# Performance work log

Measured on AMD Instinct MI355X. Metric: run time of the kernel, lower is better.

## Reference

```python
import jax, jax.numpy as jnp
import numpy as np

N, E, F_IN, D, H = 20000, 640000, 128, 16, 8  # nodes, edges, in_features, out_features, n_heads


def _linear_params(k, fan_in, fan_out):
    W = jax.random.normal(k, (fan_in, fan_out), jnp.float32) / np.sqrt(fan_in)
    b = jnp.zeros((fan_out,), jnp.float32)
    return W, b


def setup_inputs() -> dict:
    key = jax.random.key(0)
    ks = jax.random.split(key, 8)
    x = jax.random.normal(ks[0], (N, F_IN), jnp.float32)
    edge_index = jax.random.randint(ks[1], (2, E), 0, N, dtype=jnp.int64)
    Wq, bq = _linear_params(ks[2], F_IN, D * H)
    Wk, bk = _linear_params(ks[3], F_IN, D * H)
    Wv, bv = _linear_params(ks[4], F_IN, D * H)
    Wpsi, bpsi = _linear_params(ks[5], D, D)
    Wo, bo = _linear_params(ks[6], D * H * 2, F_IN)
    gamma = jnp.ones((F_IN,), jnp.float32)
    beta = jnp.zeros((F_IN,), jnp.float32)
    return {"x": x, "edge_index": edge_index, "Wq": Wq, "bq": bq, "Wk": Wk, "bk": bk,
            "Wv": Wv, "bv": bv, "Wpsi": Wpsi, "bpsi": bpsi, "Wo": Wo, "bo": bo,
            "gamma": gamma, "beta": beta}


def _segment_softmax(logits, seg, num_segments):
    # numerically-stable softmax of edge logits grouped by destination node (row)
    m = jax.ops.segment_max(logits, seg, num_segments=num_segments)  # [N,H]
    m = jnp.where(jnp.isfinite(m), m, 0.0)
    e = jnp.exp(logits - m[seg])  # [E,H]
    s = jax.ops.segment_sum(e, seg, num_segments=num_segments)  # [N,H]
    return e / (s[seg] + 1e-16)


def reference(x, edge_index, Wq, bq, Wk, bk, Wv, bv, Wpsi, bpsi, Wo, bo, gamma, beta):
    q = (x @ Wq + bq).reshape(N, H, D)
    k = (x @ Wk + bk).reshape(N, H, D)
    v = (x @ Wv + bv).reshape(N, H, D)
    row, col = edge_index[0], edge_index[1]

    logits = jnp.einsum('ehd,ehd->eh', q[row], k[col]) / np.sqrt(D)  # [E,H]
    alpha = _segment_softmax(logits, row, N)  # [E,H]

    v_j = v[col]  # [E,H,D]
    h_lp = jax.ops.segment_sum((alpha[..., None] * v_j).reshape(E, H * D), row, num_segments=N)
    v_bp = jnp.tanh(v_j @ Wpsi + bpsi)  # per-head linear on last dim, [E,H,D]
    h_bp = jax.ops.segment_sum((alpha[..., None] * v_bp).reshape(E, H * D), row, num_segments=N)

    h_out = jnp.concatenate([h_lp, h_bp], axis=1) @ Wo + bo  # [N,F_IN]
    y = x + jax.nn.relu(h_out)
    mu = jnp.mean(y, axis=-1, keepdims=True)
    var = jnp.mean(jnp.square(y - mu), axis=-1, keepdims=True)
    return (y - mu) * jax.lax.rsqrt(var + 1e-5) * gamma + beta
```

## Files before the change

### kernel.cpp

```cpp
#include <hip/hip_runtime.h>
#include <hip/hip_bf16.h>
#include <math.h>

#define NN 20000
#define EE 640000

typedef __attribute__((ext_vector_type(8))) short short8;
typedef __attribute__((ext_vector_type(4))) float f32x4;
typedef __hip_bfloat16 bf16;
typedef __hip_bfloat162 bf162;

__device__ inline ushort f2bf(float f) {
  bf16 h = __float2bfloat16(f);
  return *(ushort*)&h;
}
__device__ inline float2 bf2u(uint u) {
  return __bfloat1622float2(*(const bf162*)&u);
}
__device__ inline float fast_tanh(float x) {
  float xx = fminf(fmaxf(x, -9.0f), 9.0f);
  float e = exp2f(xx * 2.885390082f);
  return (e - 1.0f) * __builtin_amdgcn_rcpf(e + 1.0f);
}
__device__ inline short8 frag_from_f32(const float* p) {
  float4 f0 = *(const float4*)p;
  float4 f1 = *(const float4*)(p + 4);
  ushort tmp[8] = {f2bf(f0.x), f2bf(f0.y), f2bf(f0.z), f2bf(f0.w),
                   f2bf(f1.x), f2bf(f1.y), f2bf(f1.z), f2bf(f1.w)};
  return *(const short8*)tmp;
}


__global__ __launch_bounds__(256, 4) void qkv_gemm(
    const float* __restrict__ x,
    const float* __restrict__ Wq, const float* __restrict__ bq,
    const float* __restrict__ Wk, const float* __restrict__ bk,
    const float* __restrict__ Wv, const float* __restrict__ bv,
    float* __restrict__ qbuf,
    ushort* __restrict__ kbuf, ushort* __restrict__ vbuf) {
  __shared__ ushort WB[128 * 136];
  int t = threadIdx.x;
  int n0 = blockIdx.x * 128;
  int mat = blockIdx.y;
  const float* W    = mat == 0 ? Wq : (mat == 1 ? Wk : Wv);
  const float* bias = mat == 0 ? bq : (mat == 1 ? bk : bv);

  {
    int k = t >> 1, nh = (t & 1) * 64;
    const float* src = W + (size_t)k * 128 + nh;
#pragma unroll
    for (int i = 0; i < 16; ++i) {
      float4 f = *(const float4*)(src + 4 * i);
      WB[(nh + 4 * i + 0) * 136 + k] = f2bf(f.x);
      WB[(nh + 4 * i + 1) * 136 + k] = f2bf(f.y);
      WB[(nh + 4 * i + 2) * 136 + k] = f2bf(f.z);
      WB[(nh + 4 * i + 3) * 136 + k] = f2bf(f.w);
    }
  }
  __syncthreads();

  int w = t >> 6, lane = t & 63;
  int m = lane & 15, q = lane >> 4;
  int r0 = w * 32;
  int row0 = n0 + r0 + m;
  int row1 = row0 + 16;
  bool ok0 = row0 < NN, ok1 = row1 < NN;
  const float* xr0 = x + (size_t)row0 * 128;
  const float* xr1 = x + (size_t)row1 * 128;
  const short8 z8 = (short8){0, 0, 0, 0, 0, 0, 0, 0};

  f32x4 acc0[8], acc1[8];
#pragma unroll
  for (int c = 0; c < 8; ++c) {
    acc0[c] = (f32x4){0.f, 0.f, 0.f, 0.f};
    acc1[c] = (f32x4){0.f, 0.f, 0.f, 0.f};
  }
#pragma unroll
  for (int kt = 0; kt < 4; ++kt) {
    int kof = kt * 32 + 8 * q;
    short8 a0 = ok0 ? frag_from_f32(xr0 + kof) : z8;
    short8 a1 = ok1 ? frag_from_f32(xr1 + kof) : z8;
#pragma unroll
    for (int c = 0; c < 8; ++c) {
      short8 b = *(const short8*)&WB[(c * 16 + m) * 136 + kof];
      acc0[c] = __builtin_amdgcn_mfma_f32_16x16x32_bf16(a0, b, acc0[c], 0, 0, 0);
      acc1[c] = __builtin_amdgcn_mfma_f32_16x16x32_bf16(a1, b, acc1[c], 0, 0, 0);
    }
  }
  if (mat == 0) {
#pragma unroll
    for (int c = 0; c < 8; ++c) {
      int col = c * 16 + m;
      float bb = bias[col];
#pragma unroll
      for (int reg = 0; reg < 4; ++reg) {
        int ra = n0 + r0 + 4 * q + reg;
        int rb = ra + 16;
        if (ra < NN) qbuf[(size_t)ra * 128 + col] = acc0[c][reg] + bb;
        if (rb < NN) qbuf[(size_t)rb * 128 + col] = acc1[c][reg] + bb;
      }
    }
  } else {
    ushort* dst = (mat == 1) ? kbuf : vbuf;
#pragma unroll
    for (int c = 0; c < 8; ++c) {
      int col = c * 16 + m;
      float bb = bias[col];
#pragma unroll
      for (int reg = 0; reg < 4; ++reg) {
        int ra = n0 + r0 + 4 * q + reg;
        int rb = ra + 16;
        if (ra < NN) dst[(size_t)ra * 128 + col] = f2bf(acc0[c][reg] + bb);
        if (rb < NN) dst[(size_t)rb * 128 + col] = f2bf(acc1[c][reg] + bb);
      }
    }
  }
}

__global__ __launch_bounds__(256) void vb_kernel(
    const ushort* __restrict__ vbuf, ushort* __restrict__ bbuf,
    const float* __restrict__ Wpsi, const float* __restrict__ bpsi) {
  __shared__ float Ws[256];
  __shared__ float bs[16];
  int t = threadIdx.x;
  Ws[t] = Wpsi[t];
  if (t < 16) bs[t] = bpsi[t];
  __syncthreads();
  int idx = blockIdx.x * 256 + t;
  int n = idx >> 3, h = idx & 7;
  const ushort* vp = vbuf + (size_t)n * 128 + h * 16;
  uint4 a = *(const uint4*)vp;
  uint4 b = *(const uint4*)(vp + 8);
  float v[16];
  {
    float2 f;
    f = bf2u(a.x); v[0] = f.x;  v[1] = f.y;
    f = bf2u(a.y); v[2] = f.x;  v[3] = f.y;
    f = bf2u(a.z); v[4] = f.x;  v[5] = f.y;
    f = bf2u(a.w); v[6] = f.x;  v[7] = f.y;
    f = bf2u(b.x); v[8] = f.x;  v[9] = f.y;
    f = bf2u(b.y); v[10] = f.x; v[11] = f.y;
    f = bf2u(b.z); v[12] = f.x; v[13] = f.y;
    f = bf2u(b.w); v[14] = f.x; v[15] = f.y;
  }
  float o[16];
#pragma unroll
  for (int d = 0; d < 16; ++d) o[d] = bs[d];
#pragma unroll
  for (int dp = 0; dp < 16; ++dp) {
    float vv = v[dp];
#pragma unroll
    for (int d = 0; d < 16; ++d) o[d] = fmaf(vv, Ws[dp * 16 + d], o[d]);
  }
  ushort* dst = bbuf + (size_t)n * 128 + h * 16;
  uint u[8];
#pragma unroll
  for (int j = 0; j < 8; ++j)
    u[j] = (uint)f2bf(fast_tanh(o[2 * j])) |
           ((uint)f2bf(fast_tanh(o[2 * j + 1])) << 16);
  *(uint4*)dst = *(const uint4*)&u[0];
  *(uint4*)(dst + 8) = *(const uint4*)&u[4];
}

__global__ __launch_bounds__(256) void scatter_kernel(
    const int* __restrict__ ei,
    int* __restrict__ cursor, ushort* __restrict__ scol) {
  int e = blockIdx.x * 256 + threadIdx.x;
  if (e < EE) {
    int r = ei[e];
    int c = ei[EE + e];
    int pos = atomicAdd(&cursor[r], 1);
    if (pos < 128) scol[r * 128 + pos] = (ushort)c;
  }
}

__global__ __launch_bounds__(256) void aggregate_kernel(
    const float* __restrict__ qbuf,
    const ushort* __restrict__ kbuf, const ushort* __restrict__ vbuf,
    const ushort* __restrict__ bbuf,
    const int* __restrict__ cursor, const ushort* __restrict__ scol,
    ushort* __restrict__ hbufb) {
  int wid = threadIdx.x >> 6, lane = threadIdx.x & 63;
  int node = blockIdx.x * 4 + wid;
  int h = lane >> 3, dg = (lane & 7) * 2;
  int off = h * 16 + dg;
  const float SC = 0.25f * 1.44269504f;
  float2 q2 = *(const float2*)(qbuf + (size_t)node * 128 + off);
  q2.x *= SC; q2.y *= SC;
  int cnt = cursor[node];
  cnt = cnt > 128 ? 128 : cnt;
  const ushort* srow = scol + node * 128;
  float s = 0.f, aV0 = 0.f, aV1 = 0.f, aB0 = 0.f, aB1 = 0.f;

  auto proc1 = [&](uint K, uint V, uint B) {
    float2 kk = bf2u(K);
    float d = fmaf(q2.x, kk.x, q2.y * kk.y);
    d += __shfl_xor(d, 1);
    d += __shfl_xor(d, 2);
    d += __shfl_xor(d, 4);
    float wgt = exp2f(d);
    s += wgt;
    float2 vv = bf2u(V);
    aV0 = fmaf(wgt, vv.x, aV0); aV1 = fmaf(wgt, vv.y, aV1);
    float2 tb = bf2u(B);
    aB0 = fmaf(wgt, tb.x, aB0); aB1 = fmaf(wgt, tb.y, aB1);
  };

  int i = 0;
  for (; i + 8 <= cnt; i += 8) {
    uint4 wv = *(const uint4*)(srow + i);
    int id[8] = {(int)(wv.x & 0xffffu), (int)(wv.x >> 16),
                 (int)(wv.y & 0xffffu), (int)(wv.y >> 16),
                 (int)(wv.z & 0xffffu), (int)(wv.z >> 16),
                 (int)(wv.w & 0xffffu), (int)(wv.w >> 16)};
    uint K[8], V[8], B[8];
#pragma unroll
    for (int j = 0; j < 8; ++j) {
      size_t base = (size_t)id[j] * 128 + off;
      K[j] = *(const uint*)(kbuf + base);
      V[j] = *(const uint*)(vbuf + base);
      B[j] = *(const uint*)(bbuf + base);
    }
#pragma unroll
    for (int j = 0; j < 8; ++j) proc1(K[j], V[j], B[j]);
  }
  for (; i < cnt; ++i) {
    int e = srow[i];
    size_t base = (size_t)e * 128 + off;
    proc1(*(const uint*)(kbuf + base), *(const uint*)(vbuf + base),
          *(const uint*)(bbuf + base));
  }

  float inv = s > 0.f ? 1.f / s : 0.f;
  ushort* hp = hbufb + (size_t)node * 256 + off;
  uint uv = (uint)f2bf(aV0 * inv) | ((uint)f2bf(aV1 * inv) << 16);
  uint ub = (uint)f2bf(aB0 * inv) | ((uint)f2bf(aB1 * inv) << 16);
  *(uint*)(hp)       = uv;
  *(uint*)(hp + 128) = ub;
}

__global__ __launch_bounds__(256, 4) void output_mfma(
    const ushort* __restrict__ hbufb, const float* __restrict__ x,
    const float* __restrict__ Wo, const float* __restrict__ bo,
    const float* __restrict__ gamma, const float* __restrict__ beta,
    float* __restrict__ out) {
  __shared__ ushort WB[128 * 136];
  __shared__ float bos[128], gs[128], bts[128];
  int t = threadIdx.x;
  int n0 = blockIdx.x * 128;
  if (t < 128) { bos[t] = bo[t]; gs[t] = gamma[t]; bts[t] = beta[t]; }
  int w = t >> 6, lane = t & 63;
  int m = lane & 15, q = lane >> 4;
  int r0 = w * 32;
  int row0 = n0 + r0 + m;
  int row1 = row0 + 16;
  bool ok0 = row0 < NN, ok1 = row1 < NN;
  const ushort* hr0 = hbufb + (size_t)row0 * 256;
  const ushort* hr1 = hbufb + (size_t)row1 * 256;
  const short8 z8 = (short8){0, 0, 0, 0, 0, 0, 0, 0};

  f32x4 acc0[8], acc1[8];
#pragma unroll
  for (int c = 0; c < 8; ++c) {
    acc0[c] = (f32x4){0.f, 0.f, 0.f, 0.f};
    acc1[c] = (f32x4){0.f, 0.f, 0.f, 0.f};
  }
  for (int kc = 0; kc < 2; ++kc) {
    if (kc) __syncthreads();
    {
      int k = t >> 1, nh = (t & 1) * 64;
      const float* src = Wo + (size_t)(kc * 128 + k) * 128 + nh;
#pragma unroll
      for (int i = 0; i < 16; ++i) {
        float4 f = *(const float4*)(src + 4 * i);
        WB[(nh + 4 * i + 0) * 136 + k] = f2bf(f.x);
        WB[(nh + 4 * i + 1) * 136 + k] = f2bf(f.y);
        WB[(nh + 4 * i + 2) * 136 + k] = f2bf(f.z);
        WB[(nh + 4 * i + 3) * 136 + k] = f2bf(f.w);
      }
    }
    __syncthreads();
#pragma unroll
    for (int kt = 0; kt < 4; ++kt) {
      int kof = kt * 32 + 8 * q;
      short8 a0 = ok0 ? *(const short8*)(hr0 + kc * 128 + kof) : z8;
      short8 a1 = ok1 ? *(const short8*)(hr1 + kc * 128 + kof) : z8;
#pragma unroll
      for (int c = 0; c < 8; ++c) {
        short8 b = *(const short8*)&WB[(c * 16 + m) * 136 + kof];
        acc0[c] = __builtin_amdgcn_mfma_f32_16x16x32_bf16(a0, b, acc0[c], 0, 0, 0);
        acc1[c] = __builtin_amdgcn_mfma_f32_16x16x32_bf16(a1, b, acc1[c], 0, 0, 0);
      }
    }
  }
#pragma unroll
  for (int half = 0; half < 2; ++half) {
#pragma unroll
    for (int reg = 0; reg < 4; ++reg) {
      int row = n0 + r0 + half * 16 + 4 * q + reg;
      bool valid = row < NN;
      float vals[8];
      float sum = 0.f;
#pragma unroll
      for (int c = 0; c < 8; ++c) {
        int col = c * 16 + m;
        float a = (half ? acc1[c][reg] : acc0[c][reg]) + bos[col];
        a = fmaxf(a, 0.f);
        float xv = valid ? x[(size_t)row * 128 + col] : 0.f;
        float v = a + xv;
        vals[c] = v;
        sum += v;
      }
      sum += __shfl_xor(sum, 1); sum += __shfl_xor(sum, 2);
      sum += __shfl_xor(sum, 4); sum += __shfl_xor(sum, 8);
      float mean = sum * (1.f / 128.f);
      float ssq = 0.f;
#pragma unroll
      for (int c = 0; c < 8; ++c) {
        float d = vals[c] - mean;
        ssq = fmaf(d, d, ssq);
      }
      ssq += __shfl_xor(ssq, 1); ssq += __shfl_xor(ssq, 2);
      ssq += __shfl_xor(ssq, 4); ssq += __shfl_xor(ssq, 8);
      float rstd = rsqrtf(ssq * (1.f / 128.f) + 1e-5f);
      if (valid) {
#pragma unroll
        for (int c = 0; c < 8; ++c) {
          int col = c * 16 + m;
          out[(size_t)row * 128 + col] = (vals[c] - mean) * rstd * gs[col] + bts[col];
        }
      }
    }
  }
}

extern "C" void kernel_launch(void* const* d_in, const int* in_sizes, int n_in,
                              void* d_out, int out_size, void* d_ws, size_t ws_size,
                              hipStream_t stream) {
  const float* x     = (const float*)d_in[0];
  const int*   ei    = (const int*)d_in[1];
  const float* Wq    = (const float*)d_in[2];
  const float* bq    = (const float*)d_in[3];
  const float* Wk    = (const float*)d_in[4];
  const float* bk    = (const float*)d_in[5];
  const float* Wv    = (const float*)d_in[6];
  const float* bv    = (const float*)d_in[7];
  const float* Wpsi  = (const float*)d_in[8];
  const float* bpsi  = (const float*)d_in[9];
  const float* Wo    = (const float*)d_in[10];
  const float* bo    = (const float*)d_in[11];
  const float* gamma = (const float*)d_in[12];
  const float* beta  = (const float*)d_in[13];
  float* out = (float*)d_out;

  char* ws = (char*)d_ws;
  float*  qbuf   = (float*) (ws);
  ushort* kbuf   = (ushort*)(ws + 10240000);
  ushort* vbuf   = (ushort*)(ws + 15360000);
  ushort* bbuf   = (ushort*)(ws + 20480000);
  ushort* hbufb  = (ushort*)(ws + 25600000);
  int*    cursor = (int*)   (ws + 35840000);
  ushort* scol   = (ushort*)(ws + 35920000);

  hipMemsetAsync(cursor, 0, 80000, stream);

  qkv_gemm<<<dim3(157, 3), 256, 0, stream>>>(x, Wq, bq, Wk, bk, Wv, bv,
                                             qbuf, kbuf, vbuf);
  vb_kernel<<<625, 256, 0, stream>>>(vbuf, bbuf, Wpsi, bpsi);
  scatter_kernel<<<2500, 256, 0, stream>>>(ei, cursor, scol);
  aggregate_kernel<<<5000, 256, 0, stream>>>(qbuf, kbuf, vbuf, bbuf,
                                             cursor, scol, hbufb);
  output_mfma<<<157, 256, 0, stream>>>(hbufb, x, Wo, bo, gamma, beta, out);
}
```

Baseline: 222.9 us.

## Bucket neighbor lists by source-column chunk via count-then-scan CSR build

Edge counts per (row, column-chunk) bucket are now computed inside the QKV GEMM kernel, prefix-summed per node in vb_kernel, and then used by the scatter kernel to place neighbors grouped by source-column range. Grouping each node's neighbor list by column chunk should improve the locality of K/V/B gathers in aggregation and spread atomics across more addresses. In exchange it adds an extra pass over the edge list with atomics and a larger memset, and neighbor ordering changes (clipping at 128 is now per-bucket offset, which may drop different edges if degree exceeds 128).

```diff
diff --git a/kernel.cpp b/kernel.cpp
--- a/kernel.cpp
+++ b/kernel.cpp
@@ -4,6 +4,8 @@
 
 #define NN 20000
 #define EE 640000
+#define NCH 16
+#define CHN 1250
 
 typedef __attribute__((ext_vector_type(8))) short short8;
 typedef __attribute__((ext_vector_type(4))) float f32x4;
@@ -36,12 +38,24 @@
     const float* __restrict__ Wq, const float* __restrict__ bq,
     const float* __restrict__ Wk, const float* __restrict__ bk,
     const float* __restrict__ Wv, const float* __restrict__ bv,
+    const int* __restrict__ ei,
     float* __restrict__ qbuf,
-    ushort* __restrict__ kbuf, ushort* __restrict__ vbuf) {
+    ushort* __restrict__ kbuf, ushort* __restrict__ vbuf,
+    int* __restrict__ cnt2) {
   __shared__ ushort WB[128 * 136];
   int t = threadIdx.x;
   int n0 = blockIdx.x * 128;
   int mat = blockIdx.y;
+
+  {
+    int flat = (mat * 157 + blockIdx.x) * 256 + t;
+    for (int e = flat; e < EE; e += 157 * 3 * 256) {
+      int r = ei[e];
+      int c = ei[EE + e];
+      atomicAdd(&cnt2[r * NCH + c / CHN], 1);
+    }
+  }
+
   const float* W    = mat == 0 ? Wq : (mat == 1 ? Wk : Wv);
   const float* bias = mat == 0 ? bq : (mat == 1 ? bk : bv);
 
@@ -119,7 +133,8 @@
 
 __global__ __launch_bounds__(256) void vb_kernel(
     const ushort* __restrict__ vbuf, ushort* __restrict__ bbuf,
-    const float* __restrict__ Wpsi, const float* __restrict__ bpsi) {
+    const float* __restrict__ Wpsi, const float* __restrict__ bpsi,
+    int* __restrict__ cnt2, int* __restrict__ cursor) {
   __shared__ float Ws[256];
   __shared__ float bs[16];
   int t = threadIdx.x;
@@ -127,6 +142,19 @@
   if (t < 16) bs[t] = bpsi[t];
   __syncthreads();
   int idx = blockIdx.x * 256 + t;
+
+  if (idx < NN) {
+    int* p = cnt2 + idx * NCH;
+    int run = 0;
+#pragma unroll
+    for (int j = 0; j < NCH; ++j) {
+      int v = p[j];
+      p[j] = run;
+      run += v;
+    }
+    cursor[idx] = run > 128 ? 128 : run;
+  }
+
   int n = idx >> 3, h = idx & 7;
   const ushort* vp = vbuf + (size_t)n * 128 + h * 16;
   uint4 a = *(const uint4*)vp;
@@ -164,12 +192,12 @@
 
 __global__ __launch_bounds__(256) void scatter_kernel(
     const int* __restrict__ ei,
-    int* __restrict__ cursor, ushort* __restrict__ scol) {
+    int* __restrict__ cnt2, ushort* __restrict__ scol) {
   int e = blockIdx.x * 256 + threadIdx.x;
   if (e < EE) {
     int r = ei[e];
     int c = ei[EE + e];
-    int pos = atomicAdd(&cursor[r], 1);
+    int pos = atomicAdd(&cnt2[r * NCH + c / CHN], 1);
     if (pos < 128) scol[r * 128 + pos] = (ushort)c;
   }
 }
@@ -188,7 +216,6 @@
   float2 q2 = *(const float2*)(qbuf + (size_t)node * 128 + off);
   q2.x *= SC; q2.y *= SC;
   int cnt = cursor[node];
-  cnt = cnt > 128 ? 128 : cnt;
   const ushort* srow = scol + node * 128;
   float s = 0.f, aV0 = 0.f, aV1 = 0.f, aB0 = 0.f, aB1 = 0.f;
 
@@ -360,14 +387,15 @@
   ushort* bbuf   = (ushort*)(ws + 20480000);
   ushort* hbufb  = (ushort*)(ws + 25600000);
   int*    cursor = (int*)   (ws + 35840000);
-  ushort* scol   = (ushort*)(ws + 35920000);
-
-  hipMemsetAsync(cursor, 0, 80000, stream);
-
-  qkv_gemm<<<dim3(157, 3), 256, 0, stream>>>(x, Wq, bq, Wk, bk, Wv, bv,
-                                             qbuf, kbuf, vbuf);
-  vb_kernel<<<625, 256, 0, stream>>>(vbuf, bbuf, Wpsi, bpsi);
-  scatter_kernel<<<2500, 256, 0, stream>>>(ei, cursor, scol);
+  int*    cnt2   = (int*)   (ws + 35920000);
+  ushort* scol   = (ushort*)(ws + 37200000);
+
+  hipMemsetAsync(cnt2, 0, 1280000, stream);
+
+  qkv_gemm<<<dim3(157, 3), 256, 0, stream>>>(x, Wq, bq, Wk, bk, Wv, bv, ei,
+                                             qbuf, kbuf, vbuf, cnt2);
+  vb_kernel<<<625, 256, 0, stream>>>(vbuf, bbuf, Wpsi, bpsi, cnt2, cursor);
+  scatter_kernel<<<2500, 256, 0, stream>>>(ei, cnt2, scol);
   aggregate_kernel<<<5000, 256, 0, stream>>>(qbuf, kbuf, vbuf, bbuf,
                                              cursor, scol, hbufb);
   output_mfma<<<157, 256, 0, stream>>>(hbufb, x, Wo, bo, gamma, beta, out);
```

Measured after the change: 246.4 us. 1.11x slower.

## Fuse edge scatter and psi projection into QKV GEMM kernel

Applied to the files above, without the earlier changes.

Folds the edge bucketing scatter and the per-head psi linear plus tanh into the QKV GEMM kernel, removing two separate launches. The scatter runs as a grid-stride loop at the start of every GEMM block. The V-matrix blocks stage their bf16 V tile in shared memory and compute the tanh projection from there, so V is not re-read from global memory. The cost is extra work and atomics inside the GEMM blocks, and some imbalance because only a third of the blocks do the psi step.

```diff
diff --git a/kernel.cpp b/kernel.cpp
--- a/kernel.cpp
+++ b/kernel.cpp
@@ -36,14 +36,35 @@
     const float* __restrict__ Wq, const float* __restrict__ bq,
     const float* __restrict__ Wk, const float* __restrict__ bk,
     const float* __restrict__ Wv, const float* __restrict__ bv,
+    const float* __restrict__ Wpsi, const float* __restrict__ bpsi,
+    const int* __restrict__ ei,
     float* __restrict__ qbuf,
-    ushort* __restrict__ kbuf, ushort* __restrict__ vbuf) {
+    ushort* __restrict__ kbuf, ushort* __restrict__ vbuf,
+    ushort* __restrict__ bbuf,
+    int* __restrict__ cursor, ushort* __restrict__ scol) {
   __shared__ ushort WB[128 * 136];
+  __shared__ float Wps[256];
+  __shared__ float bps[16];
   int t = threadIdx.x;
   int n0 = blockIdx.x * 128;
   int mat = blockIdx.y;
+
+  {
+    int flat = (mat * 157 + blockIdx.x) * 256 + t;
+    for (int e = flat; e < EE; e += 157 * 3 * 256) {
+      int r = ei[e];
+      int c = ei[EE + e];
+      int pos = atomicAdd(&cursor[r], 1);
+      if (pos < 128) scol[r * 128 + pos] = (ushort)c;
+    }
+  }
+
   const float* W    = mat == 0 ? Wq : (mat == 1 ? Wk : Wv);
   const float* bias = mat == 0 ? bq : (mat == 1 ? bk : bv);
+  if (mat == 2) {
+    Wps[t] = Wpsi[t];
+    if (t < 16) bps[t] = bpsi[t];
+  }
 
   {
     int k = t >> 1, nh = (t & 1) * 64;
@@ -102,6 +123,7 @@
     }
   } else {
     ushort* dst = (mat == 1) ? kbuf : vbuf;
+    if (mat == 2) __syncthreads();
 #pragma unroll
     for (int c = 0; c < 8; ++c) {
       int col = c * 16 + m;
@@ -110,67 +132,59 @@
       for (int reg = 0; reg < 4; ++reg) {
         int ra = n0 + r0 + 4 * q + reg;
         int rb = ra + 16;
-        if (ra < NN) dst[(size_t)ra * 128 + col] = f2bf(acc0[c][reg] + bb);
-        if (rb < NN) dst[(size_t)rb * 128 + col] = f2bf(acc1[c][reg] + bb);
-      }
-    }
-  }
-}
-
-__global__ __launch_bounds__(256) void vb_kernel(
-    const ushort* __restrict__ vbuf, ushort* __restrict__ bbuf,
-    const float* __restrict__ Wpsi, const float* __restrict__ bpsi) {
-  __shared__ float Ws[256];
-  __shared__ float bs[16];
-  int t = threadIdx.x;
-  Ws[t] = Wpsi[t];
-  if (t < 16) bs[t] = bpsi[t];
-  __syncthreads();
-  int idx = blockIdx.x * 256 + t;
-  int n = idx >> 3, h = idx & 7;
-  const ushort* vp = vbuf + (size_t)n * 128 + h * 16;
-  uint4 a = *(const uint4*)vp;
-  uint4 b = *(const uint4*)(vp + 8);
-  float v[16];
-  {
-    float2 f;
-    f = bf2u(a.x); v[0] = f.x;  v[1] = f.y;
-    f = bf2u(a.y); v[2] = f.x;  v[3] = f.y;
-    f = bf2u(a.z); v[4] = f.x;  v[5] = f.y;
-    f = bf2u(a.w); v[6] = f.x;  v[7] = f.y;
-    f = bf2u(b.x); v[8] = f.x;  v[9] = f.y;
-    f = bf2u(b.y); v[10] = f.x; v[11] = f.y;
-    f = bf2u(b.z); v[12] = f.x; v[13] = f.y;
-    f = bf2u(b.w); v[14] = f.x; v[15] = f.y;
-  }
-  float o[16];
-#pragma unroll
-  for (int d = 0; d < 16; ++d) o[d] = bs[d];
-#pragma unroll
-  for (int dp = 0; dp < 16; ++dp) {
-    float vv = v[dp];
-#pragma unroll
-    for (int d = 0; d < 16; ++d) o[d] = fmaf(vv, Ws[dp * 16 + d], o[d]);
-  }
-  ushort* dst = bbuf + (size_t)n * 128 + h * 16;
-  uint u[8];
-#pragma unroll
-  for (int j = 0; j < 8; ++j)
-    u[j] = (uint)f2bf(fast_tanh(o[2 * j])) |
-           ((uint)f2bf(fast_tanh(o[2 * j + 1])) << 16);
-  *(uint4*)dst = *(const uint4*)&u[0];
-  *(uint4*)(dst + 8) = *(const uint4*)&u[4];
-}
-
-__global__ __launch_bounds__(256) void scatter_kernel(
-    const int* __restrict__ ei,
-    int* __restrict__ cursor, ushort* __restrict__ scol) {
-  int e = blockIdx.x * 256 + threadIdx.x;
-  if (e < EE) {
-    int r = ei[e];
-    int c = ei[EE + e];
-    int pos = atomicAdd(&cursor[r], 1);
-    if (pos < 128) scol[r * 128 + pos] = (ushort)c;
+        ushort h0 = f2bf(acc0[c][reg] + bb);
+        ushort h1 = f2bf(acc1[c][reg] + bb);
+        if (ra < NN) dst[(size_t)ra * 128 + col] = h0;
+        if (rb < NN) dst[(size_t)rb * 128 + col] = h1;
+        if (mat == 2) {
+          WB[(r0 + 4 * q + reg) * 136 + col] = h0;
+          WB[(r0 + 16 + 4 * q + reg) * 136 + col] = h1;
+        }
+      }
+    }
+    if (mat == 2) {
+      __syncthreads();
+#pragma unroll
+      for (int ii = 0; ii < 4; ++ii) {
+        int cell = ii * 256 + t;
+        int rl = cell >> 3, h = cell & 7;
+        int n = n0 + rl;
+        const ushort* vp = &WB[rl * 136 + h * 16];
+        uint4 a = *(const uint4*)vp;
+        uint4 b = *(const uint4*)(vp + 8);
+        float v[16];
+        {
+          float2 f;
+          f = bf2u(a.x); v[0] = f.x;  v[1] = f.y;
+          f = bf2u(a.y); v[2] = f.x;  v[3] = f.y;
+          f = bf2u(a.z); v[4] = f.x;  v[5] = f.y;
+          f = bf2u(a.w); v[6] = f.x;  v[7] = f.y;
+          f = bf2u(b.x); v[8] = f.x;  v[9] = f.y;
+          f = bf2u(b.y); v[10] = f.x; v[11] = f.y;
+          f = bf2u(b.z); v[12] = f.x; v[13] = f.y;
+          f = bf2u(b.w); v[14] = f.x; v[15] = f.y;
+        }
+        float o[16];
+#pragma unroll
+        for (int d = 0; d < 16; ++d) o[d] = bps[d];
+#pragma unroll
+        for (int dp = 0; dp < 16; ++dp) {
+          float vv = v[dp];
+#pragma unroll
+          for (int d = 0; d < 16; ++d) o[d] = fmaf(vv, Wps[dp * 16 + d], o[d]);
+        }
+        if (n < NN) {
+          ushort* db = bbuf + (size_t)n * 128 + h * 16;
+          uint u[8];
+#pragma unroll
+          for (int j = 0; j < 8; ++j)
+            u[j] = (uint)f2bf(fast_tanh(o[2 * j])) |
+                   ((uint)f2bf(fast_tanh(o[2 * j + 1])) << 16);
+          *(uint4*)db = *(const uint4*)&u[0];
+          *(uint4*)(db + 8) = *(const uint4*)&u[4];
+        }
+      }
+    }
   }
 }
 
@@ -365,9 +379,8 @@
   hipMemsetAsync(cursor, 0, 80000, stream);
 
   qkv_gemm<<<dim3(157, 3), 256, 0, stream>>>(x, Wq, bq, Wk, bk, Wv, bv,
-                                             qbuf, kbuf, vbuf);
-  vb_kernel<<<625, 256, 0, stream>>>(vbuf, bbuf, Wpsi, bpsi);
-  scatter_kernel<<<2500, 256, 0, stream>>>(ei, cursor, scol);
+                                             Wpsi, bpsi, ei, qbuf,
+                                             kbuf, vbuf, bbuf, cursor, scol);
   aggregate_kernel<<<5000, 256, 0, stream>>>(qbuf, kbuf, vbuf, bbuf,
                                              cursor, scol, hbufb);
   output_mfma<<<157, 256, 0, stream>>>(hbufb, x, Wo, bo, gamma, beta, out);
```

New measurement: 222.8 us. Within noise of the previous version (-0.0%).
